# Kernel tuning notes

Measured on AMD Instinct MI355X. Metric: run time of the kernel, lower is better.

## Reference

```python
import jax, jax.numpy as jnp
import numpy as np

N_NODES = 80000
N_EDGES = 1280000
IN_CH = 128
HID = 64
N_GRAPHS = 64
DROPOUT_P = 0.3


def setup_inputs() -> dict:
    key = jax.random.key(0)
    ks = jax.random.split(key, 12)
    x = jax.random.normal(ks[0], (N_NODES, IN_CH), dtype=jnp.float32)
    edge_index = jax.random.randint(ks[1], (2, N_EDGES), 0, N_NODES, dtype=jnp.int64 if jax.config.read('jax_enable_x64') else jnp.int32)
    batch = jnp.sort(jax.random.randint(ks[2], (N_NODES,), 0, N_GRAPHS))
    def lin(k, fan_in, fan_out):
        lim = 1.0 / np.sqrt(fan_in)
        kw, kb = jax.random.split(k)
        W = jax.random.uniform(kw, (fan_in, fan_out), minval=-lim, maxval=lim, dtype=jnp.float32)
        b = jax.random.uniform(kb, (fan_out,), minval=-lim, maxval=lim, dtype=jnp.float32)
        return W, b
    W1, b1 = lin(ks[3], IN_CH, HID)
    W2, b2 = lin(ks[4], HID, HID)
    W3, b3 = lin(ks[5], HID, HID)
    Wm1, bm1 = lin(ks[6], HID, HID)
    Wm2, bm2 = lin(ks[7], HID, 1)
    return {"x": x, "edge_index": edge_index, "batch": batch,
            "W1": W1, "b1": b1, "W2": W2, "b2": b2, "W3": W3, "b3": b3,
            "Wm1": Wm1, "bm1": bm1, "Wm2": Wm2, "bm2": bm2}


def _gcn_conv(x, W, b, src, dst, deg_inv_sqrt):
    # PyG GCNConv: h = X W; add self-loops; norm_e = d^-1/2[src] * d^-1/2[dst]
    h = x @ W  # [N, F]
    norm = deg_inv_sqrt[src] * deg_inv_sqrt[dst]  # [E]
    agg = jax.ops.segment_sum(h[src] * norm[:, None], dst, num_segments=x.shape[0])
    agg = agg + h * (deg_inv_sqrt * deg_inv_sqrt)[:, None]  # self-loop term d^-1
    return agg + b


def _dropout(x, key, p):
    keep = jax.random.bernoulli(key, 1.0 - p, x.shape)
    return jnp.where(keep, x / (1.0 - p), 0.0)


def reference(x, edge_index, batch, W1, b1, W2, b2, W3, b3, Wm1, bm1, Wm2, bm2):
    src, dst = edge_index[0], edge_index[1]
    N = x.shape[0]
    # in-degree on dst, +1 for self-loop (PyG default normalization)
    deg = jax.ops.segment_sum(jnp.ones_like(dst, dtype=x.dtype), dst, num_segments=N) + 1.0
    deg_inv_sqrt = jax.lax.rsqrt(deg)

    dk = jax.random.split(jax.random.key(42), 4)
    h = _dropout(jax.nn.relu(_gcn_conv(x, W1, b1, src, dst, deg_inv_sqrt)), dk[0], DROPOUT_P)
    h = _dropout(jax.nn.relu(_gcn_conv(h, W2, b2, src, dst, deg_inv_sqrt)), dk[1], DROPOUT_P)
    h = _dropout(jax.nn.relu(_gcn_conv(h, W3, b3, src, dst, deg_inv_sqrt)), dk[2], DROPOUT_P)

    # global mean pool per graph
    sums = jax.ops.segment_sum(h, batch, num_segments=N_GRAPHS)
    counts = jax.ops.segment_sum(jnp.ones((N,), dtype=h.dtype), batch, num_segments=N_GRAPHS)
    pooled = sums / jnp.maximum(counts, 1.0)[:, None]  # [G, HID]

    # MLP head: Linear -> ReLU -> Dropout -> Linear
    m = jax.nn.relu(pooled @ Wm1 + bm1)
    m = _dropout(m, dk[3], DROPOUT_P)
    return m @ Wm2 + bm2  # [G, 1]
```

## Files before the change

kernel.cpp:

```cpp
#include <hip/hip_runtime.h>
#include <hip/hip_fp8.h>
#include <stdint.h>

#define HID 64
#define INCH 128
#define NGRAPH 64
#define KEEPP 0.7f
#define SCAN_B 256

typedef __attribute__((ext_vector_type(8))) short short8;
typedef __attribute__((ext_vector_type(4))) float floatx4;
typedef __attribute__((ext_vector_type(2))) float floatx2;
typedef unsigned short ushort_t;

__device__ __forceinline__ uint8_t f2e4(float f) {
  __hip_fp8_e4m3 t(f);
  return (uint8_t)t.__x;
}
__device__ __forceinline__ float e42f(uint8_t b) {
  __hip_fp8_e4m3 t;
  t.__x = (__hip_fp8_storage_t)b;
  return (float)t;
}

__device__ __forceinline__ void e42f_x4(uint32_t r, float& f0, float& f1,
                                        float& f2, float& f3) {
#if __has_builtin(__builtin_amdgcn_cvt_pk_f32_fp8)
  floatx2 lo = __builtin_amdgcn_cvt_pk_f32_fp8((int)r, false);
  floatx2 hi = __builtin_amdgcn_cvt_pk_f32_fp8((int)r, true);
  f0 = lo.x; f1 = lo.y; f2 = hi.x; f3 = hi.y;
#else
  f0 = e42f((uint8_t)(r      ));
  f1 = e42f((uint8_t)(r >>  8));
  f2 = e42f((uint8_t)(r >> 16));
  f3 = e42f((uint8_t)(r >> 24));
#endif
}

__host__ __device__ inline void tf2x32(uint32_t k0, uint32_t k1,
                                       uint32_t& x0, uint32_t& x1) {
  const uint32_t ks2 = k0 ^ k1 ^ 0x1BD11BDAu;
#define ROTL32(v, d) (((v) << (d)) | ((v) >> (32 - (d))))
#define TF_RND(r) { x0 += x1; x1 = ROTL32(x1, r); x1 ^= x0; }
  x0 += k0; x1 += k1;
  TF_RND(13) TF_RND(15) TF_RND(26) TF_RND(6)
  x0 += k1;  x1 += ks2 + 1u;
  TF_RND(17) TF_RND(29) TF_RND(16) TF_RND(24)
  x0 += ks2; x1 += k0 + 2u;
  TF_RND(13) TF_RND(15) TF_RND(26) TF_RND(6)
  x0 += k0;  x1 += k1 + 3u;
  TF_RND(17) TF_RND(29) TF_RND(16) TF_RND(24)
  x0 += k1;  x1 += ks2 + 4u;
  TF_RND(13) TF_RND(15) TF_RND(26) TF_RND(6)
  x0 += ks2; x1 += k0 + 5u;
#undef TF_RND
#undef ROTL32
}

__device__ __forceinline__ bool keep_mask(uint32_t k0, uint32_t k1, uint32_t idx) {
  uint32_t x0 = 0u, x1 = idx;
  tf2x32(k0, k1, x0, x1);
  uint32_t bits = x0 ^ x1;
  float u = __uint_as_float((bits >> 9) | 0x3f800000u) - 1.0f;
  return u < KEEPP;
}

__global__ void k_hist(const int* __restrict__ dst, int E, int* __restrict__ counts) {
  int e = blockIdx.x * blockDim.x + threadIdx.x;
  if (e < E) atomicAdd(&counts[dst[e]], 1);
}

__global__ __launch_bounds__(SCAN_B) void k_scan1d(const int* __restrict__ counts,
                                                   int* __restrict__ bsum,
                                                   float* __restrict__ dinv,
                                                   const int* __restrict__ batch,
                                                   float* __restrict__ cnts, int N) {
  __shared__ int lh[NGRAPH];
  if (threadIdx.x < NGRAPH) lh[threadIdx.x] = 0;
  __syncthreads();
  int i = blockIdx.x * SCAN_B + threadIdx.x;
  int v = 0;
  if (i < N) {
    v = counts[i];
    dinv[i] = rsqrtf((float)v + 1.0f);
    atomicAdd(&lh[batch[i]], 1);
  }
  int r = v;
  for (int off = 32; off > 0; off >>= 1) r += __shfl_down(r, off);
  __shared__ int ws[4];
  if ((threadIdx.x & 63) == 0) ws[threadIdx.x >> 6] = r;
  __syncthreads();
  if (threadIdx.x == 0) bsum[blockIdx.x] = ws[0] + ws[1] + ws[2] + ws[3];
  if (threadIdx.x < NGRAPH && lh[threadIdx.x] != 0)
    atomicAdd(&cnts[threadIdx.x], (float)lh[threadIdx.x]);
}

__device__ __forceinline__ void wsplit_one(const float* __restrict__ W,
                                           short8* __restrict__ Wh,
                                           short8* __restrict__ Wl, int i) {
  int lane = i & 63, f = i >> 6;
  int kc = f >> 2, ct = f & 3;
  int kbase = kc * 32 + ((lane >> 4) << 3);
  int n = ct * 16 + (lane & 15);
  short8 h, l;
#pragma unroll
  for (int j = 0; j < 8; ++j) {
    float w = W[(size_t)(kbase + j) * HID + n];
    uint32_t u = __float_as_uint(w);
    h[j] = (short)(u >> 16);
    float r = w - __uint_as_float(u & 0xFFFF0000u);
    l[j] = (short)(__float_as_uint(r) >> 16);
  }
  Wh[i] = h;
  Wl[i] = l;
}

__global__ __launch_bounds__(1024) void k_scan2w(const int* __restrict__ bsum,
                                                 int* __restrict__ bpre, int B,
                                                 float* __restrict__ sums,
                                                 const float* __restrict__ W1,
                                                 short8* __restrict__ Wh1, short8* __restrict__ Wl1,
                                                 const float* __restrict__ W2,
                                                 short8* __restrict__ Wh2, short8* __restrict__ Wl2,
                                                 const float* __restrict__ W3,
                                                 short8* __restrict__ Wh3, short8* __restrict__ Wl3) {
  if (blockIdx.x == 0) {
    __shared__ int s[1024];
    int tid = threadIdx.x;
    for (int i = tid; i < NGRAPH * HID; i += 1024) sums[i] = 0.0f;
    int v = (tid < B) ? bsum[tid] : 0;
    s[tid] = v;
    __syncthreads();
    for (int off = 1; off < 1024; off <<= 1) {
      int t = (tid >= off) ? s[tid - off] : 0;
      __syncthreads();
      s[tid] += t;
      __syncthreads();
    }
    if (tid < B) bpre[tid] = s[tid] - v;
    return;
  }
  int b = blockIdx.x - 1;
  int tid = threadIdx.x;
  if (b == 0) {
    wsplit_one(W1, Wh1, Wl1, tid);
  } else if (b == 1 && tid < 512) {
    wsplit_one(W2, Wh2, Wl2, tid);
  } else if (b == 2 && tid < 512) {
    wsplit_one(W3, Wh3, Wl3, tid);
  }
}

__global__ __launch_bounds__(SCAN_B) void k_scan3(const int* __restrict__ counts,
                                                  const int* __restrict__ bpre,
                                                  int* __restrict__ row_off,
                                                  int* __restrict__ cursor,
                                                  int N, int E) {
  __shared__ int s[SCAN_B];
  int tid = threadIdx.x;
  int i = blockIdx.x * SCAN_B + tid;
  int v = (i < N) ? counts[i] : 0;
  s[tid] = v;
  __syncthreads();
  for (int off = 1; off < SCAN_B; off <<= 1) {
    int t = (tid >= off) ? s[tid - off] : 0;
    __syncthreads();
    s[tid] += t;
    __syncthreads();
  }
  if (i < N) {
    int excl = bpre[blockIdx.x] + s[tid] - v;
    row_off[i] = excl;
    cursor[i] = excl;
  }
  if (i == 0) row_off[N] = E;
}

template <int K>
__device__ __forceinline__ void mgemm_tile(const float* __restrict__ A,
                                           const short8* __restrict__ Wh,
                                           const short8* __restrict__ Wl,
                                           uint8_t* __restrict__ C, int N,
                                           int tile) {
  constexpr int KC = K / 32;
  const int lane = threadIdx.x & 63;
  const int wv = threadIdx.x >> 6;
  const int m = lane & 15;
  const int q = lane >> 4;
  const int row0 = tile * 64 + wv * 16;
  if (row0 >= N) return;
  const int arow = min(row0 + m, N - 1);
  const float* __restrict__ ap = A + (size_t)arow * K + (q << 3);

  floatx4 acc[4];
#pragma unroll
  for (int ct = 0; ct < 4; ++ct) acc[ct] = (floatx4){0.f, 0.f, 0.f, 0.f};

#pragma unroll
  for (int kc = 0; kc < KC; ++kc) {
    const floatx4* apv = (const floatx4*)(ap + kc * 32);
    floatx4 x0 = apv[0];
    floatx4 x1 = apv[1];
    short8 ah, al;
#pragma unroll
    for (int j = 0; j < 4; ++j) {
      uint32_t u = __float_as_uint(x0[j]);
      ah[j] = (short)(u >> 16);
      float r = x0[j] - __uint_as_float(u & 0xFFFF0000u);
      al[j] = (short)(__float_as_uint(r) >> 16);
    }
#pragma unroll
    for (int j = 0; j < 4; ++j) {
      uint32_t u = __float_as_uint(x1[j]);
      ah[4 + j] = (short)(u >> 16);
      float r = x1[j] - __uint_as_float(u & 0xFFFF0000u);
      al[4 + j] = (short)(__float_as_uint(r) >> 16);
    }
#pragma unroll
    for (int ct = 0; ct < 4; ++ct) {
      short8 bh = Wh[(kc * 4 + ct) * 64 + lane];
      short8 bl = Wl[(kc * 4 + ct) * 64 + lane];
      acc[ct] = __builtin_amdgcn_mfma_f32_16x16x32_bf16(ah, bh, acc[ct], 0, 0, 0);
      acc[ct] = __builtin_amdgcn_mfma_f32_16x16x32_bf16(ah, bl, acc[ct], 0, 0, 0);
      acc[ct] = __builtin_amdgcn_mfma_f32_16x16x32_bf16(al, bh, acc[ct], 0, 0, 0);
    }
  }

  uint8_t* __restrict__ cp = C + (size_t)row0 * HID;
#pragma unroll
  for (int ct = 0; ct < 4; ++ct)
#pragma unroll
    for (int r = 0; r < 4; ++r) {
      int rr = (q << 2) + r;
      if (row0 + rr < N) cp[(size_t)rr * HID + ct * 16 + m] = f2e4(acc[ct][r]);
    }
}

template <int K>
__global__ __launch_bounds__(256) void k_mgemm_build(
    const float* __restrict__ A, const short8* __restrict__ Wh,
    const short8* __restrict__ Wl, uint8_t* __restrict__ C, int N,
    const int* __restrict__ src, const int* __restrict__ dst,
    const float* __restrict__ dinv, int* __restrict__ cursor,
    int2* __restrict__ csr, int E, int build_blocks, int gemm_blocks) {
  const long T = (long)build_blocks + gemm_blocks;
  const long b = (long)blockIdx.x;
  const long gb = (b * gemm_blocks) / T;
  const bool is_g = (((b + 1) * gemm_blocks) / T) != gb;
  if (!is_g) {
    int bb = (int)(b - gb);
    int e = bb * 256 + (int)threadIdx.x;
    if (e < E) {
      int s = src[e], d = dst[e];
      int pos = atomicAdd(&cursor[d], 1);
      csr[pos] = make_int2(s, __float_as_int(dinv[s] * dinv[d]));
    }
    return;
  }
  mgemm_tile<K>(A, Wh, Wl, C, N, (int)gb);
}

template <int K>
__global__ __launch_bounds__(256) void k_mgemm(const float* __restrict__ A,
                                               const short8* __restrict__ Wh,
                                               const short8* __restrict__ Wl,
                                               uint8_t* __restrict__ C, int N) {
  mgemm_tile<K>(A, Wh, Wl, C, N, (int)blockIdx.x);
}

__device__ __forceinline__ float gather_core(const uint8_t* __restrict__ tmp,
                                             const int2* __restrict__ csr,
                                             int beg, int end, int q, int sl) {
  float a0 = 0.f, a1 = 0.f, a2 = 0.f, a3 = 0.f;
  for (int j = beg; j < end; j += 8) {
    int e0 = j + q, e1 = j + 4 + q;
    bool v0 = e0 < end, v1 = e1 < end;
    int2 p0 = csr[v0 ? e0 : beg];
    int2 p1 = csr[v1 ? e1 : beg];
    float w0 = v0 ? __int_as_float(p0.y) : 0.0f;
    float w1 = v1 ? __int_as_float(p1.y) : 0.0f;
    uint32_t r0 = *(const uint32_t*)(tmp + (size_t)p0.x * HID + sl * 4);
    uint32_t r1 = *(const uint32_t*)(tmp + (size_t)p1.x * HID + sl * 4);
    float f0, f1, f2, f3, g0, g1, g2, g3;
    e42f_x4(r0, f0, f1, f2, f3);
    e42f_x4(r1, g0, g1, g2, g3);
    a0 = fmaf(f0, w0, a0); a1 = fmaf(f1, w0, a1);
    a2 = fmaf(f2, w0, a2); a3 = fmaf(f3, w0, a3);
    a0 = fmaf(g0, w1, a0); a1 = fmaf(g1, w1, a1);
    a2 = fmaf(g2, w1, a2); a3 = fmaf(g3, w1, a3);
  }
  a0 += __shfl_xor(a0, 16); a0 += __shfl_xor(a0, 32);
  a1 += __shfl_xor(a1, 16); a1 += __shfl_xor(a1, 32);
  a2 += __shfl_xor(a2, 16); a2 += __shfl_xor(a2, 32);
  a3 += __shfl_xor(a3, 16); a3 += __shfl_xor(a3, 32);
  return (q == 0) ? a0 : (q == 1) ? a1 : (q == 2) ? a2 : a3;
}

__global__ __launch_bounds__(256) void k_gather(const uint8_t* __restrict__ tmp,
                                                const int* __restrict__ row_off,
                                                const int2* __restrict__ csr,
                                                const float* __restrict__ dinv,
                                                const float* __restrict__ bias,
                                                float* __restrict__ outh, int N,
                                                uint32_t k0, uint32_t k1) {
  const int node = blockIdx.x * 4 + (threadIdx.x >> 6);
  const int lane = threadIdx.x & 63;
  const int q = lane >> 4;
  const int sl = lane & 15;
  if (node >= N) return;
  const int beg = __builtin_amdgcn_readfirstlane(row_off[node]);
  const int end = __builtin_amdgcn_readfirstlane(row_off[node + 1]);
  float acc = gather_core(tmp, csr, beg, end, q, sl);
  const int ch = sl * 4 + q;
  const float dnode = dinv[node];
  const int idx = node * HID + ch;
  float v = acc + e42f(tmp[(size_t)node * HID + ch]) * dnode * dnode + bias[ch];
  v = fmaxf(v, 0.0f);
  v = keep_mask(k0, k1, (uint32_t)idx) ? v / KEEPP : 0.0f;
  outh[idx] = v;
}

__global__ __launch_bounds__(256) void k_pool(const float* __restrict__ h,
                                              const int* __restrict__ batch,
                                              float* __restrict__ sums, int N) {
  __shared__ float ls[NGRAPH * HID];
  for (int i = threadIdx.x; i < NGRAPH * HID; i += 256) ls[i] = 0.0f;
  __syncthreads();
  const int lane = threadIdx.x & 63;
  const int wave = threadIdx.x >> 6;
  int per = (N + gridDim.x - 1) / gridDim.x;
  int beg = blockIdx.x * per;
  int end = min(N, beg + per);
  for (int i = beg + wave; i < end; i += 4) {
    int g = batch[i];
    atomicAdd(&ls[g * HID + lane], h[(size_t)i * HID + lane]);
  }
  __syncthreads();
  for (int i = threadIdx.x; i < NGRAPH * HID; i += 256)
    if (ls[i] != 0.0f) atomicAdd(&sums[i], ls[i]);
}

__global__ __launch_bounds__(256) void k_head(const float* __restrict__ sums,
                                              const float* __restrict__ cnts,
                                              const float* __restrict__ Wm1,
                                              const float* __restrict__ bm1,
                                              const float* __restrict__ Wm2,
                                              const float* __restrict__ bm2,
                                              float* __restrict__ out,
                                              uint32_t k0, uint32_t k1) {
  __shared__ float pooled[NGRAPH * HID];
  __shared__ float m[NGRAPH * HID];
  for (int i = threadIdx.x; i < NGRAPH * HID; i += 256) {
    int g = i >> 6;
    pooled[i] = sums[i] / fmaxf(cnts[g], 1.0f);
  }
  __syncthreads();
  for (int i = threadIdx.x; i < NGRAPH * HID; i += 256) {
    int g = i >> 6, j = i & 63;
    float acc = bm1[j];
#pragma unroll 8
    for (int k = 0; k < HID; ++k)
      acc = fmaf(pooled[g * HID + k], Wm1[k * HID + j], acc);
    acc = fmaxf(acc, 0.0f);
    m[i] = keep_mask(k0, k1, (uint32_t)i) ? acc / KEEPP : 0.0f;
  }
  __syncthreads();
  if (threadIdx.x < NGRAPH) {
    int g = threadIdx.x;
    float acc = bm2[0];
#pragma unroll 8
    for (int j = 0; j < HID; ++j)
      acc = fmaf(m[g * HID + j], Wm2[j], acc);
    out[g] = acc;
  }
}

extern "C" void kernel_launch(void* const* d_in, const int* in_sizes, int n_in,
                              void* d_out, int out_size, void* d_ws, size_t ws_size,
                              hipStream_t stream) {
  const float* x     = (const float*)d_in[0];
  const int*   ei    = (const int*)d_in[1];
  const int*   batch = (const int*)d_in[2];
  const float* W1 = (const float*)d_in[3];
  const float* b1 = (const float*)d_in[4];
  const float* W2 = (const float*)d_in[5];
  const float* b2 = (const float*)d_in[6];
  const float* W3 = (const float*)d_in[7];
  const float* b3 = (const float*)d_in[8];
  const float* Wm1 = (const float*)d_in[9];
  const float* bm1 = (const float*)d_in[10];
  const float* Wm2 = (const float*)d_in[11];
  const float* bm2 = (const float*)d_in[12];
  float* out = (float*)d_out;

  const int N = in_sizes[0] / INCH;
  const int E = in_sizes[1] / 2;
  const int* src = ei;
  const int* dst = ei + E;
  const int NB = (N + SCAN_B - 1) / SCAN_B;

  char* ws = (char*)d_ws;
  size_t off = 0;
  uint8_t* B0 = (uint8_t*)(ws + off); off += (size_t)N * HID;
  off = (off + 15) & ~(size_t)15;
  float* B1      = (float*)(ws + off); off += (size_t)N * HID * 4;
  int*   counts  = (int*)  (ws + off); off += (size_t)N * 4;
  float* cnts    = (float*)(ws + off); off += NGRAPH * 4;
  float* dinv    = (float*)(ws + off); off += (size_t)N * 4;
  int*   row_off = (int*)  (ws + off); off += ((size_t)N + 4) * 4;
  int*   cursor  = (int*)  (ws + off); off += (size_t)N * 4;
  int*   bsum    = (int*)  (ws + off); off += 1024 * 4;
  int*   bpre    = (int*)  (ws + off); off += 1024 * 4;
  int2*  csr     = (int2*) (ws + off); off += (size_t)E * 8;
  float* sums    = (float*)(ws + off); off += NGRAPH * HID * 4;
  off = (off + 15) & ~(size_t)15;
  short8* Wh1 = (short8*)(ws + off); off += 1024 * 16;
  short8* Wl1 = (short8*)(ws + off); off += 1024 * 16;
  short8* Wh2 = (short8*)(ws + off); off += 512 * 16;
  short8* Wl2 = (short8*)(ws + off); off += 512 * 16;
  short8* Wh3 = (short8*)(ws + off); off += 512 * 16;
  short8* Wl3 = (short8*)(ws + off); off += 512 * 16;

  uint32_t dk[4][2];
  for (uint32_t i = 0; i < 4; ++i) {
    uint32_t a = 0u, b = i;
    tf2x32(0u, 42u, a, b);
    dk[i][0] = a; dk[i][1] = b;
  }

  hipMemsetAsync(counts, 0, ((size_t)N + NGRAPH) * sizeof(int), stream);
  k_hist<<<(E + 255) / 256, 256, 0, stream>>>(dst, E, counts);
  k_scan1d<<<NB, SCAN_B, 0, stream>>>(counts, bsum, dinv, batch, cnts, N);
  k_scan2w<<<4, 1024, 0, stream>>>(bsum, bpre, NB, sums,
                                   W1, Wh1, Wl1, W2, Wh2, Wl2, W3, Wh3, Wl3);
  k_scan3<<<NB, SCAN_B, 0, stream>>>(counts, bpre, row_off, cursor, N, E);

  const int build_grid = (E + 255) / 256;
  const int mg_grid    = (N + 63) / 64;
  const int gath_grid  = (N + 3) / 4;

  k_mgemm_build<INCH><<<build_grid + mg_grid, 256, 0, stream>>>(
      x, Wh1, Wl1, B0, N, src, dst, dinv, cursor, csr, E, build_grid, mg_grid);
  k_gather<<<gath_grid, 256, 0, stream>>>(B0, row_off, csr, dinv, b1,
                                          B1, N, dk[0][0], dk[0][1]);
  k_mgemm<HID><<<mg_grid, 256, 0, stream>>>(B1, Wh2, Wl2, B0, N);
  k_gather<<<gath_grid, 256, 0, stream>>>(B0, row_off, csr, dinv, b2,
                                          B1, N, dk[1][0], dk[1][1]);
  k_mgemm<HID><<<mg_grid, 256, 0, stream>>>(B1, Wh3, Wl3, B0, N);
  k_gather<<<gath_grid, 256, 0, stream>>>(B0, row_off, csr, dinv, b3,
                                          B1, N, dk[2][0], dk[2][1]);

  k_pool<<<256, 256, 0, stream>>>(B1, batch, sums, N);
  k_head<<<1, 256, 0, stream>>>(sums, cnts, Wm1, bm1, Wm2, bm2, out,
                                dk[3][0], dk[3][1]);
  (void)n_in; (void)out_size; (void)ws_size;
}
```

Before: 411.6 us.

## Fuse gather with next-layer GEMM and add nontemporal loads

Layers 1 and 2 now run a single kernel that aggregates each node's neighbours, applies bias, ReLU and dropout, stages the 64-row tile in shared memory, and multiplies it by the next weight matrix with MFMA, writing fp8 output. This drops the fp32 intermediate round trip through global memory and two kernel launches, using ping-pong fp8 buffers. Each block now gathers 16 nodes per wave sequentially instead of one node per wave, which lowers parallelism in the latency-bound gather. The CSR entries are packed into uint64 and several streaming loads and stores become nontemporal.

New measurement: 465.5 us. 13.1% more time.

```diff
diff --git a/kernel.cpp b/kernel.cpp
--- a/kernel.cpp
+++ b/kernel.cpp
@@ -11,7 +11,6 @@
 typedef __attribute__((ext_vector_type(8))) short short8;
 typedef __attribute__((ext_vector_type(4))) float floatx4;
 typedef __attribute__((ext_vector_type(2))) float floatx2;
-typedef unsigned short ushort_t;
 
 __device__ __forceinline__ uint8_t f2e4(float f) {
   __hip_fp8_e4m3 t(f);
@@ -22,7 +21,6 @@
   t.__x = (__hip_fp8_storage_t)b;
   return (float)t;
 }
-
 __device__ __forceinline__ void e42f_x4(uint32_t r, float& f0, float& f1,
                                         float& f2, float& f3) {
 #if __has_builtin(__builtin_amdgcn_cvt_pk_f32_fp8)
@@ -67,7 +65,7 @@
 
 __global__ void k_hist(const int* __restrict__ dst, int E, int* __restrict__ counts) {
   int e = blockIdx.x * blockDim.x + threadIdx.x;
-  if (e < E) atomicAdd(&counts[dst[e]], 1);
+  if (e < E) atomicAdd(&counts[__builtin_nontemporal_load(dst + e)], 1);
 }
 
 __global__ __launch_bounds__(SCAN_B) void k_scan1d(const int* __restrict__ counts,
@@ -177,72 +175,12 @@
 }
 
 template <int K>
-__device__ __forceinline__ void mgemm_tile(const float* __restrict__ A,
-                                           const short8* __restrict__ Wh,
-                                           const short8* __restrict__ Wl,
-                                           uint8_t* __restrict__ C, int N,
-                                           int tile) {
-  constexpr int KC = K / 32;
-  const int lane = threadIdx.x & 63;
-  const int wv = threadIdx.x >> 6;
-  const int m = lane & 15;
-  const int q = lane >> 4;
-  const int row0 = tile * 64 + wv * 16;
-  if (row0 >= N) return;
-  const int arow = min(row0 + m, N - 1);
-  const float* __restrict__ ap = A + (size_t)arow * K + (q << 3);
-
-  floatx4 acc[4];
-#pragma unroll
-  for (int ct = 0; ct < 4; ++ct) acc[ct] = (floatx4){0.f, 0.f, 0.f, 0.f};
-
-#pragma unroll
-  for (int kc = 0; kc < KC; ++kc) {
-    const floatx4* apv = (const floatx4*)(ap + kc * 32);
-    floatx4 x0 = apv[0];
-    floatx4 x1 = apv[1];
-    short8 ah, al;
-#pragma unroll
-    for (int j = 0; j < 4; ++j) {
-      uint32_t u = __float_as_uint(x0[j]);
-      ah[j] = (short)(u >> 16);
-      float r = x0[j] - __uint_as_float(u & 0xFFFF0000u);
-      al[j] = (short)(__float_as_uint(r) >> 16);
-    }
-#pragma unroll
-    for (int j = 0; j < 4; ++j) {
-      uint32_t u = __float_as_uint(x1[j]);
-      ah[4 + j] = (short)(u >> 16);
-      float r = x1[j] - __uint_as_float(u & 0xFFFF0000u);
-      al[4 + j] = (short)(__float_as_uint(r) >> 16);
-    }
-#pragma unroll
-    for (int ct = 0; ct < 4; ++ct) {
-      short8 bh = Wh[(kc * 4 + ct) * 64 + lane];
-      short8 bl = Wl[(kc * 4 + ct) * 64 + lane];
-      acc[ct] = __builtin_amdgcn_mfma_f32_16x16x32_bf16(ah, bh, acc[ct], 0, 0, 0);
-      acc[ct] = __builtin_amdgcn_mfma_f32_16x16x32_bf16(ah, bl, acc[ct], 0, 0, 0);
-      acc[ct] = __builtin_amdgcn_mfma_f32_16x16x32_bf16(al, bh, acc[ct], 0, 0, 0);
-    }
-  }
-
-  uint8_t* __restrict__ cp = C + (size_t)row0 * HID;
-#pragma unroll
-  for (int ct = 0; ct < 4; ++ct)
-#pragma unroll
-    for (int r = 0; r < 4; ++r) {
-      int rr = (q << 2) + r;
-      if (row0 + rr < N) cp[(size_t)rr * HID + ct * 16 + m] = f2e4(acc[ct][r]);
-    }
-}
-
-template <int K>
 __global__ __launch_bounds__(256) void k_mgemm_build(
     const float* __restrict__ A, const short8* __restrict__ Wh,
     const short8* __restrict__ Wl, uint8_t* __restrict__ C, int N,
     const int* __restrict__ src, const int* __restrict__ dst,
     const float* __restrict__ dinv, int* __restrict__ cursor,
-    int2* __restrict__ csr, int E, int build_blocks, int gemm_blocks) {
+    uint64_t* __restrict__ csr, int E, int build_blocks, int gemm_blocks) {
   const long T = (long)build_blocks + gemm_blocks;
   const long b = (long)blockIdx.x;
   const long gb = (b * gemm_blocks) / T;
@@ -251,36 +189,81 @@
     int bb = (int)(b - gb);
     int e = bb * 256 + (int)threadIdx.x;
     if (e < E) {
-      int s = src[e], d = dst[e];
+      int s = __builtin_nontemporal_load(src + e);
+      int d = __builtin_nontemporal_load(dst + e);
       int pos = atomicAdd(&cursor[d], 1);
-      csr[pos] = make_int2(s, __float_as_int(dinv[s] * dinv[d]));
+      uint32_t w = __float_as_uint(dinv[s] * dinv[d]);
+      csr[pos] = ((uint64_t)w << 32) | (uint32_t)s;
     }
     return;
   }
-  mgemm_tile<K>(A, Wh, Wl, C, N, (int)gb);
-}
-
-template <int K>
-__global__ __launch_bounds__(256) void k_mgemm(const float* __restrict__ A,
-                                               const short8* __restrict__ Wh,
-                                               const short8* __restrict__ Wl,
-                                               uint8_t* __restrict__ C, int N) {
-  mgemm_tile<K>(A, Wh, Wl, C, N, (int)blockIdx.x);
+  constexpr int KC = K / 32;
+  const int lane = threadIdx.x & 63;
+  const int wv = threadIdx.x >> 6;
+  const int m = lane & 15;
+  const int q = lane >> 4;
+  const int row0 = (int)gb * 64 + wv * 16;
+  if (row0 >= N) return;
+  const int arow = min(row0 + m, N - 1);
+  const float* __restrict__ ap = A + (size_t)arow * K + (q << 3);
+
+  floatx4 acc[4];
+#pragma unroll
+  for (int ct = 0; ct < 4; ++ct) acc[ct] = (floatx4){0.f, 0.f, 0.f, 0.f};
+
+#pragma unroll
+  for (int kc = 0; kc < KC; ++kc) {
+    const floatx4* apv = (const floatx4*)(ap + kc * 32);
+    floatx4 x0 = __builtin_nontemporal_load(apv);
+    floatx4 x1 = __builtin_nontemporal_load(apv + 1);
+    short8 ah, al;
+#pragma unroll
+    for (int j = 0; j < 4; ++j) {
+      uint32_t u = __float_as_uint(x0[j]);
+      ah[j] = (short)(u >> 16);
+      float r = x0[j] - __uint_as_float(u & 0xFFFF0000u);
+      al[j] = (short)(__float_as_uint(r) >> 16);
+    }
+#pragma unroll
+    for (int j = 0; j < 4; ++j) {
+      uint32_t u = __float_as_uint(x1[j]);
+      ah[4 + j] = (short)(u >> 16);
+      float r = x1[j] - __uint_as_float(u & 0xFFFF0000u);
+      al[4 + j] = (short)(__float_as_uint(r) >> 16);
+    }
+#pragma unroll
+    for (int ct = 0; ct < 4; ++ct) {
+      short8 bh = Wh[(kc * 4 + ct) * 64 + lane];
+      short8 bl = Wl[(kc * 4 + ct) * 64 + lane];
+      acc[ct] = __builtin_amdgcn_mfma_f32_16x16x32_bf16(ah, bh, acc[ct], 0, 0, 0);
+      acc[ct] = __builtin_amdgcn_mfma_f32_16x16x32_bf16(ah, bl, acc[ct], 0, 0, 0);
+      acc[ct] = __builtin_amdgcn_mfma_f32_16x16x32_bf16(al, bh, acc[ct], 0, 0, 0);
+    }
+  }
+
+  uint8_t* __restrict__ cp = C + (size_t)row0 * HID;
+#pragma unroll
+  for (int ct = 0; ct < 4; ++ct)
+#pragma unroll
+    for (int r = 0; r < 4; ++r) {
+      int rr = (q << 2) + r;
+      if (row0 + rr < N) cp[(size_t)rr * HID + ct * 16 + m] = f2e4(acc[ct][r]);
+    }
 }
 
 __device__ __forceinline__ float gather_core(const uint8_t* __restrict__ tmp,
-                                             const int2* __restrict__ csr,
+                                             const uint64_t* __restrict__ csr,
                                              int beg, int end, int q, int sl) {
   float a0 = 0.f, a1 = 0.f, a2 = 0.f, a3 = 0.f;
   for (int j = beg; j < end; j += 8) {
     int e0 = j + q, e1 = j + 4 + q;
     bool v0 = e0 < end, v1 = e1 < end;
-    int2 p0 = csr[v0 ? e0 : beg];
-    int2 p1 = csr[v1 ? e1 : beg];
-    float w0 = v0 ? __int_as_float(p0.y) : 0.0f;
-    float w1 = v1 ? __int_as_float(p1.y) : 0.0f;
-    uint32_t r0 = *(const uint32_t*)(tmp + (size_t)p0.x * HID + sl * 4);
-    uint32_t r1 = *(const uint32_t*)(tmp + (size_t)p1.x * HID + sl * 4);
+    uint64_t c0 = __builtin_nontemporal_load(csr + (v0 ? e0 : beg));
+    uint64_t c1 = __builtin_nontemporal_load(csr + (v1 ? e1 : beg));
+    float w0 = v0 ? __uint_as_float((uint32_t)(c0 >> 32)) : 0.0f;
+    float w1 = v1 ? __uint_as_float((uint32_t)(c1 >> 32)) : 0.0f;
+    uint32_t r0 = *(const uint32_t*)(tmp + (size_t)(uint32_t)c0 * HID + sl * 4);
+    uint32_t r1 = *(const uint32_t*)(tmp + (size_t)(uint32_t)c1 * HID + sl * 4);
     float f0, f1, f2, f3, g0, g1, g2, g3;
     e42f_x4(r0, f0, f1, f2, f3);
     e42f_x4(r1, g0, g1, g2, g3);
@@ -296,9 +279,73 @@
   return (q == 0) ? a0 : (q == 1) ? a1 : (q == 2) ? a2 : a3;
 }
 
+__global__ __launch_bounds__(256) void k_gather_gemm(
+    const uint8_t* __restrict__ tin, const int* __restrict__ row_off,
+    const uint64_t* __restrict__ csr, const float* __restrict__ dinv,
+    const float* __restrict__ bias, const short8* __restrict__ Wh,
+    const short8* __restrict__ Wl, uint8_t* __restrict__ tout, int N,
+    uint32_t k0, uint32_t k1) {
+  __shared__ float hs[64][68];
+  const int lane = threadIdx.x & 63;
+  const int wv = threadIdx.x >> 6;
+  const int q = lane >> 4;
+  const int sl = lane & 15;
+  const int row0 = blockIdx.x * 64 + wv * 16;
+  if (row0 >= N) return;
+
+  const int ch = sl * 4 + q;
+#pragma unroll 1
+  for (int i = 0; i < 16; ++i) {
+    int node = row0 + i;
+    if (node >= N) break;
+    int beg = __builtin_amdgcn_readfirstlane(row_off[node]);
+    int end = __builtin_amdgcn_readfirstlane(row_off[node + 1]);
+    float acc = gather_core(tin, csr, beg, end, q, sl);
+    float dnode = dinv[node];
+    int idx = node * HID + ch;
+    float v = acc + e42f(tin[idx]) * dnode * dnode + bias[ch];
+    v = fmaxf(v, 0.0f);
+    v = keep_mask(k0, k1, (uint32_t)idx) ? v / KEEPP : 0.0f;
+    hs[wv * 16 + i][ch] = v;
+  }
+
+  floatx4 acc[4];
+#pragma unroll
+  for (int ct = 0; ct < 4; ++ct) acc[ct] = (floatx4){0.f, 0.f, 0.f, 0.f};
+#pragma unroll
+  for (int kc = 0; kc < 2; ++kc) {
+    const float* hp = &hs[wv * 16 + sl][kc * 32 + q * 8];
+    short8 ah, al;
+#pragma unroll
+    for (int j = 0; j < 8; ++j) {
+      float xv = hp[j];
+      uint32_t u = __float_as_uint(xv);
+      ah[j] = (short)(u >> 16);
+      float r = xv - __uint_as_float(u & 0xFFFF0000u);
+      al[j] = (short)(__float_as_uint(r) >> 16);
+    }
+#pragma unroll
+    for (int ct = 0; ct < 4; ++ct) {
+      short8 bh = Wh[(kc * 4 + ct) * 64 + lane];
+      short8 bl = Wl[(kc * 4 + ct) * 64 + lane];
+      acc[ct] = __builtin_amdgcn_mfma_f32_16x16x32_bf16(ah, bh, acc[ct], 0, 0, 0);
+      acc[ct] = __builtin_amdgcn_mfma_f32_16x16x32_bf16(ah, bl, acc[ct], 0, 0, 0);
+      acc[ct] = __builtin_amdgcn_mfma_f32_16x16x32_bf16(al, bh, acc[ct], 0, 0, 0);
+    }
+  }
+  uint8_t* __restrict__ cp = tout + (size_t)row0 * HID;
+#pragma unroll
+  for (int ct = 0; ct < 4; ++ct)
+#pragma unroll
+    for (int r = 0; r < 4; ++r) {
+      int rr = (q << 2) + r;
+      if (row0 + rr < N) cp[(size_t)rr * HID + ct * 16 + sl] = f2e4(acc[ct][r]);
+    }
+}
+
 __global__ __launch_bounds__(256) void k_gather(const uint8_t* __restrict__ tmp,
                                                 const int* __restrict__ row_off,
-                                                const int2* __restrict__ csr,
+                                                const uint64_t* __restrict__ csr,
                                                 const float* __restrict__ dinv,
                                                 const float* __restrict__ bias,
                                                 float* __restrict__ outh, int N,
@@ -314,10 +361,10 @@
   const int ch = sl * 4 + q;
   const float dnode = dinv[node];
   const int idx = node * HID + ch;
-  float v = acc + e42f(tmp[(size_t)node * HID + ch]) * dnode * dnode + bias[ch];
+  float v = acc + e42f(tmp[idx]) * dnode * dnode + bias[ch];
   v = fmaxf(v, 0.0f);
   v = keep_mask(k0, k1, (uint32_t)idx) ? v / KEEPP : 0.0f;
-  outh[idx] = v;
+  __builtin_nontemporal_store(v, outh + idx);
 }
 
 __global__ __launch_bounds__(256) void k_pool(const float* __restrict__ h,
@@ -333,7 +380,8 @@
   int end = min(N, beg + per);
   for (int i = beg + wave; i < end; i += 4) {
     int g = batch[i];
-    atomicAdd(&ls[g * HID + lane], h[(size_t)i * HID + lane]);
+    float v = __builtin_nontemporal_load(h + (size_t)i * HID + lane);
+    atomicAdd(&ls[g * HID + lane], v);
   }
   __syncthreads();
   for (int i = threadIdx.x; i < NGRAPH * HID; i += 256)
@@ -401,7 +449,8 @@
 
   char* ws = (char*)d_ws;
   size_t off = 0;
-  uint8_t* B0 = (uint8_t*)(ws + off); off += (size_t)N * HID;
+  uint8_t* T1 = (uint8_t*)(ws + off); off += (size_t)N * HID;
+  uint8_t* T2 = (uint8_t*)(ws + off); off += (size_t)N * HID;
   off = (off + 15) & ~(size_t)15;
   float* B1      = (float*)(ws + off); off += (size_t)N * HID * 4;
   int*   counts  = (int*)  (ws + off); off += (size_t)N * 4;
@@ -411,7 +460,8 @@
   int*   cursor  = (int*)  (ws + off); off += (size_t)N * 4;
   int*   bsum    = (int*)  (ws + off); off += 1024 * 4;
   int*   bpre    = (int*)  (ws + off); off += 1024 * 4;
-  int2*  csr     = (int2*) (ws + off); off += (size_t)E * 8;
+  off = (off + 7) & ~(size_t)7;
+  uint64_t* csr  = (uint64_t*)(ws + off); off += (size_t)E * 8;
   float* sums    = (float*)(ws + off); off += NGRAPH * HID * 4;
   off = (off + 15) & ~(size_t)15;
   short8* Wh1 = (short8*)(ws + off); off += 1024 * 16;
@@ -440,14 +490,12 @@
   const int gath_grid  = (N + 3) / 4;
 
   k_mgemm_build<INCH><<<build_grid + mg_grid, 256, 0, stream>>>(
-      x, Wh1, Wl1, B0, N, src, dst, dinv, cursor, csr, E, build_grid, mg_grid);
-  k_gather<<<gath_grid, 256, 0, stream>>>(B0, row_off, csr, dinv, b1,
-                                          B1, N, dk[0][0], dk[0][1]);
-  k_mgemm<HID><<<mg_grid, 256, 0, stream>>>(B1, Wh2, Wl2, B0, N);
-  k_gather<<<gath_grid, 256, 0, stream>>>(B0, row_off, csr, dinv, b2,
-                                          B1, N, dk[1][0], dk[1][1]);
-  k_mgemm<HID><<<mg_grid, 256, 0, stream>>>(B1, Wh3, Wl3, B0, N);
-  k_gather<<<gath_grid, 256, 0, stream>>>(B0, row_off, csr, dinv, b3,
+      x, Wh1, Wl1, T1, N, src, dst, dinv, cursor, csr, E, build_grid, mg_grid);
+  k_gather_gemm<<<mg_grid, 256, 0, stream>>>(T1, row_off, csr, dinv, b1,
+                                             Wh2, Wl2, T2, N, dk[0][0], dk[0][1]);
+  k_gather_gemm<<<mg_grid, 256, 0, stream>>>(T2, row_off, csr, dinv, b2,
+                                             Wh3, Wl3, T1, N, dk[1][0], dk[1][1]);
+  k_gather<<<gath_grid, 256, 0, stream>>>(T1, row_off, csr, dinv, b3,
                                           B1, N, dk[2][0], dk[2][1]);
 
   k_pool<<<256, 256, 0, stream>>>(B1, batch, sums, N);
```
